# Kernel tuning notes

Hardware: AMD Instinct MI355X
Metric: run time of the kernel (lower is better)

## Reference

```python
import jax, jax.numpy as jnp
import numpy as np

N_QUBITS = 10
T_STEPS = 10
NDATA = 1024
DIM = 2 ** N_QUBITS
PI = float(np.pi)


def setup_inputs() -> dict:
    key = jax.random.key(0)
    k1, k2, k3, k4, k5 = jax.random.split(key, 5)
    # random complex amplitudes (normalized to unit states inside reference)
    inputs_re = jax.random.normal(k1, (NDATA, DIM), dtype=jnp.float32)
    inputs_im = jax.random.normal(k2, (NDATA, DIM), dtype=jnp.float32)
    # diffusion noise schedule diff_hs (t,) in (0,1]
    diff_hs = jax.random.uniform(k5, (T_STEPS,), dtype=jnp.float32, minval=0.1, maxval=1.0)
    # var_1 = diff_hs.repeat(3n) in torch == tile -> index k scaled by diff_hs[k % t]
    var_1 = jnp.tile(diff_hs, 3 * N_QUBITS)                                  # (3*n*t,)
    phis = (jax.random.uniform(k3, (NDATA, 3 * N_QUBITS * T_STEPS), dtype=jnp.float32)
            * (PI / 4.0) - (PI / 8.0)) * var_1[None, :]
    gs = (jax.random.uniform(k4, (NDATA, T_STEPS), dtype=jnp.float32) * 0.2 + 0.4) * diff_hs[None, :]
    return {"inputs_re": inputs_re, "inputs_im": inputs_im, "phis": phis, "gs": gs}


def _apply_1q(psi, M, i):
    """Apply per-sample 2x2 gate M (B,2,2) on qubit i (qubit 0 = MSB) to psi (B, 2**n)."""
    left = 2 ** i
    right = 2 ** (N_QUBITS - 1 - i)
    s = psi.reshape(NDATA, left, 2, right)
    s = jnp.einsum('bxy,bayc->baxc', M, s)
    return s.reshape(NDATA, DIM)


def _scramble(inputs_re, inputs_im, phis, gs):
    n, t = N_QUBITS, T_STEPS
    psi = (inputs_re + 1j * inputs_im).astype(jnp.complex64)
    psi = psi / jnp.linalg.norm(psi, axis=1, keepdims=True)  # unit input states

    # precompute sum_{i<j} z_i z_j per basis state for the diagonal RZZ product
    idx = jnp.arange(DIM)
    bits = (idx[:, None] >> jnp.arange(n - 1, -1, -1)[None, :]) & 1  # (DIM, n), qubit0=MSB
    z = 1.0 - 2.0 * bits.astype(jnp.float32)
    zsum = z.sum(axis=1)
    pairsum = 0.5 * (zsum ** 2 - n)                                   # (DIM,)
    inv = 1.0 / (2.0 * np.sqrt(float(n)))

    for tt in range(t):
        base = 3 * n * tt
        for i in range(n):
            a = phis[:, base + i]            # first RZ angle
            th = phis[:, base + n + i]       # RY angle
            b = phis[:, base + 2 * n + i]    # second RZ angle
            c = jnp.cos(0.5 * th).astype(jnp.complex64)
            s = jnp.sin(0.5 * th).astype(jnp.complex64)
            ea_m = jnp.exp(-0.5j * a); ea_p = jnp.exp(0.5j * a)
            eb_m = jnp.exp(-0.5j * b); eb_p = jnp.exp(0.5j * b)
            # M = RZ(b) @ RY(th) @ RZ(a), per sample (B,2,2)
            M = jnp.stack([
                jnp.stack([eb_m * c * ea_m, -eb_m * s * ea_p], axis=-1),
                jnp.stack([eb_p * s * ea_m,  eb_p * c * ea_p], axis=-1),
            ], axis=-2)
            psi = _apply_1q(psi, M, i)
        # all RZZ(i,j, theta) gates are diagonal with shared theta -> single fused phase
        theta = (gs[:, tt] * inv).astype(jnp.complex64)
        psi = psi * jnp.exp(-0.5j * theta[:, None] * pairsum[None, :])
    return psi


def reference(inputs_re, inputs_im, phis, gs):
    psi = _scramble(inputs_re, inputs_im, phis, gs)
    return jnp.stack([psi.real, psi.imag])  # (2, Ndata, 2**n) float32
```

## Files before the change

### kernel.cpp

```cpp
#include <hip/hip_runtime.h>

#define NQ 10
#define TS 10
#define DIM 1024
#define ND 1024
#define NR 16


template<int CTRL>
__device__ __forceinline__ float dpp_full(float x) {
    const int xi = __float_as_int(x);
    return __int_as_float(__builtin_amdgcn_update_dpp(xi, xi, CTRL, 0xF, 0xF, false));
}
__device__ __forceinline__ float dpp_xor4(float x) {
    const int xi = __float_as_int(x);
    int q = __builtin_amdgcn_update_dpp(0, xi, 0x104, 0xF, 0x5, false);
    q     = __builtin_amdgcn_update_dpp(q, xi, 0x114, 0xF, 0xA, false);
    return __int_as_float(q);
}
template<int MASK>
__device__ __forceinline__ float lshuf(float x) {
    if constexpr (MASK == 1)      return dpp_full<0xB1>(x);
    else if constexpr (MASK == 2) return dpp_full<0x4E>(x);
    else if constexpr (MASK == 4) return dpp_xor4(x);
    else if constexpr (MASK == 8) return dpp_full<0x128>(x);
    else return __shfl_xor(x, MASK, 64);
}

template <int RB>
__device__ __forceinline__ void ry_r(float* Sr, float* Si, float c, float s) {
#pragma unroll
    for (int r0 = 0; r0 < NR; ++r0) {
        if (r0 & (1 << RB)) continue;
        const int r1 = r0 | (1 << RB);
        const float x0r = Sr[r0], x1r = Sr[r1];
        const float x0i = Si[r0], x1i = Si[r1];
        Sr[r0] = c * x0r - s * x1r;
        Sr[r1] = s * x0r + c * x1r;
        Si[r0] = c * x0i - s * x1i;
        Si[r1] = s * x0i + c * x1i;
    }
}
template <int MASK>
__device__ __forceinline__ void ry_lane(int lane, float* Sr, float* Si,
                                        float c, float s) {
    const float ss = (lane & MASK) ? s : -s;
    float qr[NR], qi[NR];
#pragma unroll
    for (int r = 0; r < NR; ++r) {
        qr[r] = lshuf<MASK>(Sr[r]);
        qi[r] = lshuf<MASK>(Si[r]);
    }
#pragma unroll
    for (int r = 0; r < NR; ++r) {
        Sr[r] = c * Sr[r] + ss * qr[r];
        Si[r] = c * Si[r] + ss * qi[r];
    }
}

__global__ __launch_bounds__(64, 1) void qsim_kernel(
    const float* __restrict__ re_in, const float* __restrict__ im_in,
    const float* __restrict__ phis, const float* __restrict__ gs,
    float* __restrict__ out)
{
    const int sample = blockIdx.x;
    const int lane = threadIdx.x;

    const float* pr_in = re_in + sample * DIM;
    const float* pi_in = im_in + sample * DIM;

    float Sr[NR], Si[NR];
#pragma unroll
    for (int r = 0; r < NR; ++r) {
        Sr[r] = pr_in[r * 64 + lane];
        Si[r] = pi_in[r * 64 + lane];
    }

    const float inv = 0.15811388300841897f;
    const float* gsp = gs + sample * TS;

    float nrm = 0.f;
#pragma unroll
    for (int r = 0; r < NR; ++r) nrm += Sr[r] * Sr[r] + Si[r] * Si[r];
#pragma unroll
    for (int off = 32; off >= 1; off >>= 1) nrm += __shfl_xor(nrm, off, 64);
    const float scl = rsqrtf(nrm);
#pragma unroll
    for (int r = 0; r < NR; ++r) { Sr[r] *= scl; Si[r] *= scl; }

    float ps[NR];
#pragma unroll
    for (int r = 0; r < NR; ++r) {
        const int idx = r * 64 + lane;
        const int z = NQ - 2 * __popc(idx);
        ps[r] = 0.5f * (float)(z * z - NQ);
    }
    float bl[6];
#pragma unroll
    for (int j = 0; j < 6; ++j) bl[j] = (float)((lane >> (5 - j)) & 1);

    const float* ph = phis + sample * (3 * NQ * TS);

    float bprev[NQ];
#pragma unroll
    for (int i = 0; i < NQ; ++i) bprev[i] = 0.f;
    float kk = 0.f;

    auto apply_diag = [&](const float* v, float kcur) {
        float sv = 0.f;
#pragma unroll
        for (int i = 0; i < NQ; ++i) sv += v[i];
        float wl = 0.f;
#pragma unroll
        for (int j = 0; j < 6; ++j) wl = fmaf(bl[j], v[4 + j], wl);
        const float m = fmaf(-0.5f, sv, wl);
        const float Hm[4] = {m, m + v[1], m + v[0], m + v[0] + v[1]};
        const float L[4]  = {0.f, v[3], v[2], v[2] + v[3]};
#pragma unroll
        for (int r = 0; r < NR; ++r) {
            const float phi = fmaf(kcur, ps[r], Hm[r >> 2] + L[r & 3]);
            float sp, cp;
            __sincosf(phi, &sp, &cp);
            const float xr = Sr[r], xi = Si[r];
            Sr[r] = cp * xr - sp * xi;
            Si[r] = sp * xr + cp * xi;
        }
    };

    for (int tt = 0; tt < TS; ++tt) {
        float phs[30];
#pragma unroll
        for (int j = 0; j < 30; ++j) phs[j] = ph[30 * tt + j];

        float v[NQ];
#pragma unroll
        for (int i = 0; i < NQ; ++i) v[i] = phs[i] + bprev[i];
        apply_diag(v, kk);

        float rc[NQ], rs[NQ];
#pragma unroll
        for (int i = 0; i < NQ; ++i) __sincosf(0.5f * phs[10 + i], &rs[i], &rc[i]);

        ry_r<3>(Sr, Si, rc[0], rs[0]);
        ry_r<2>(Sr, Si, rc[1], rs[1]);
        ry_r<1>(Sr, Si, rc[2], rs[2]);
        ry_r<0>(Sr, Si, rc[3], rs[3]);
        ry_lane<32>(lane, Sr, Si, rc[4], rs[4]);
        ry_lane<16>(lane, Sr, Si, rc[5], rs[5]);
        ry_lane< 8>(lane, Sr, Si, rc[6], rs[6]);
        ry_lane< 4>(lane, Sr, Si, rc[7], rs[7]);
        ry_lane< 2>(lane, Sr, Si, rc[8], rs[8]);
        ry_lane< 1>(lane, Sr, Si, rc[9], rs[9]);

#pragma unroll
        for (int i = 0; i < NQ; ++i) bprev[i] = phs[20 + i];
        kk = -0.5f * (gsp[tt] * inv);
    }

    apply_diag(bprev, kk);

    float* outr = out + sample * DIM;
    float* outi = out + ND * DIM + sample * DIM;
#pragma unroll
    for (int r = 0; r < NR; ++r) {
        outr[r * 64 + lane] = Sr[r];
        outi[r * 64 + lane] = Si[r];
    }
}

extern "C" void kernel_launch(void* const* d_in, const int* in_sizes, int n_in,
                              void* d_out, int out_size, void* d_ws, size_t ws_size,
                              hipStream_t stream) {
    const float* re_in = (const float*)d_in[0];
    const float* im_in = (const float*)d_in[1];
    const float* phis  = (const float*)d_in[2];
    const float* gs    = (const float*)d_in[3];
    float* out = (float*)d_out;
    qsim_kernel<<<ND, 64, 0, stream>>>(re_in, im_in, phis, gs, out);
}
```

Before: 92.54 us.

## Apply RY gate layers as fp16 MFMA Kronecker-product matmuls

Replaces the per-qubit butterfly RY updates (register pairs plus DPP/shuffle lane exchanges) with two stages of 16x16x16 fp16 MFMA products. The first stage applies the tensor product of gates on qubits 0-3 and the second applies gates 4-9. The state is re-laid out to fit the MFMA fragment format, so the DPP/shuffle traffic goes away. The cost is fp16 rounding of the state and gate entries at every step, which may break accuracy tolerance, plus the work of building the gate matrices per lane.

```diff
diff --git a/kernel.cpp b/kernel.cpp
--- a/kernel.cpp
+++ b/kernel.cpp
@@ -4,58 +4,21 @@
 #define TS 10
 #define DIM 1024
 #define ND 1024
-#define NR 16
-
-
-template<int CTRL>
-__device__ __forceinline__ float dpp_full(float x) {
-    const int xi = __float_as_int(x);
-    return __int_as_float(__builtin_amdgcn_update_dpp(xi, xi, CTRL, 0xF, 0xF, false));
-}
-__device__ __forceinline__ float dpp_xor4(float x) {
-    const int xi = __float_as_int(x);
-    int q = __builtin_amdgcn_update_dpp(0, xi, 0x104, 0xF, 0x5, false);
-    q     = __builtin_amdgcn_update_dpp(q, xi, 0x114, 0xF, 0xA, false);
-    return __int_as_float(q);
-}
-template<int MASK>
-__device__ __forceinline__ float lshuf(float x) {
-    if constexpr (MASK == 1)      return dpp_full<0xB1>(x);
-    else if constexpr (MASK == 2) return dpp_full<0x4E>(x);
-    else if constexpr (MASK == 4) return dpp_xor4(x);
-    else if constexpr (MASK == 8) return dpp_full<0x128>(x);
-    else return __shfl_xor(x, MASK, 64);
-}
-
-template <int RB>
-__device__ __forceinline__ void ry_r(float* Sr, float* Si, float c, float s) {
-#pragma unroll
-    for (int r0 = 0; r0 < NR; ++r0) {
-        if (r0 & (1 << RB)) continue;
-        const int r1 = r0 | (1 << RB);
-        const float x0r = Sr[r0], x1r = Sr[r1];
-        const float x0i = Si[r0], x1i = Si[r1];
-        Sr[r0] = c * x0r - s * x1r;
-        Sr[r1] = s * x0r + c * x1r;
-        Si[r0] = c * x0i - s * x1i;
-        Si[r1] = s * x0i + c * x1i;
-    }
-}
-template <int MASK>
-__device__ __forceinline__ void ry_lane(int lane, float* Sr, float* Si,
-                                        float c, float s) {
-    const float ss = (lane & MASK) ? s : -s;
-    float qr[NR], qi[NR];
-#pragma unroll
-    for (int r = 0; r < NR; ++r) {
-        qr[r] = lshuf<MASK>(Sr[r]);
-        qi[r] = lshuf<MASK>(Si[r]);
-    }
-#pragma unroll
-    for (int r = 0; r < NR; ++r) {
-        Sr[r] = c * Sr[r] + ss * qr[r];
-        Si[r] = c * Si[r] + ss * qi[r];
-    }
+
+typedef _Float16 h4 __attribute__((ext_vector_type(4)));
+typedef float f4 __attribute__((ext_vector_type(4)));
+
+__device__ __forceinline__ f4 mfma16(h4 a, h4 b, f4 c) {
+    return __builtin_amdgcn_mfma_f32_16x16x16f16(a, b, c, 0, 0, 0);
+}
+__device__ __forceinline__ h4 cvt_h4(f4 x) {
+    h4 r;
+    r[0] = (_Float16)x[0]; r[1] = (_Float16)x[1];
+    r[2] = (_Float16)x[2]; r[3] = (_Float16)x[3];
+    return r;
+}
+__device__ __forceinline__ float hsel(int ob, int ib, float cq, float sq) {
+    return (ob == ib) ? cq : (ob ? sq : -sq);
 }
 
 __global__ __launch_bounds__(64, 1) void qsim_kernel(
@@ -65,41 +28,54 @@
 {
     const int sample = blockIdx.x;
     const int lane = threadIdx.x;
+    const int quad = lane >> 4;
+    const int cc = lane & 15;
+    const int c3 = (cc >> 3) & 1, c2 = (cc >> 2) & 1, c1 = (cc >> 1) & 1, c0 = cc & 1;
+    const int q1 = quad >> 1, q0 = quad & 1;
 
     const float* pr_in = re_in + sample * DIM;
     const float* pi_in = im_in + sample * DIM;
-
-    float Sr[NR], Si[NR];
-#pragma unroll
-    for (int r = 0; r < NR; ++r) {
-        Sr[r] = pr_in[r * 64 + lane];
-        Si[r] = pi_in[r * 64 + lane];
-    }
+    const float* ph = phis + sample * (3 * NQ * TS);
+    const float* gsp = gs + sample * TS;
+
+    f4 Sr[4], Si[4];
+    const int lbase = 256 * quad + cc;
+#pragma unroll
+    for (int n = 0; n < 4; ++n)
+#pragma unroll
+        for (int s = 0; s < 4; ++s) {
+            Sr[n][s] = pr_in[lbase + 64 * s + 16 * n];
+            Si[n][s] = pi_in[lbase + 64 * s + 16 * n];
+        }
 
     const float inv = 0.15811388300841897f;
-    const float* gsp = gs + sample * TS;
+    float gk[TS];
+#pragma unroll
+    for (int t = 0; t < TS; ++t) gk[t] = -0.5f * (gsp[t] * inv);
 
     float nrm = 0.f;
 #pragma unroll
-    for (int r = 0; r < NR; ++r) nrm += Sr[r] * Sr[r] + Si[r] * Si[r];
+    for (int n = 0; n < 4; ++n)
+#pragma unroll
+        for (int s = 0; s < 4; ++s) nrm += Sr[n][s] * Sr[n][s] + Si[n][s] * Si[n][s];
 #pragma unroll
     for (int off = 32; off >= 1; off >>= 1) nrm += __shfl_xor(nrm, off, 64);
     const float scl = rsqrtf(nrm);
 #pragma unroll
-    for (int r = 0; r < NR; ++r) { Sr[r] *= scl; Si[r] *= scl; }
-
-    float ps[NR];
-#pragma unroll
-    for (int r = 0; r < NR; ++r) {
-        const int idx = r * 64 + lane;
-        const int z = NQ - 2 * __popc(idx);
-        ps[r] = 0.5f * (float)(z * z - NQ);
-    }
-    float bl[6];
-#pragma unroll
-    for (int j = 0; j < 6; ++j) bl[j] = (float)((lane >> (5 - j)) & 1);
-
-    const float* ph = phis + sample * (3 * NQ * TS);
+    for (int n = 0; n < 4; ++n) { Sr[n] *= scl; Si[n] *= scl; }
+
+    float psv[4][4];
+    const int pbase = __popc(quad) + __popc(cc);
+#pragma unroll
+    for (int n = 0; n < 4; ++n)
+#pragma unroll
+        for (int s = 0; s < 4; ++s) {
+            const int p = pbase + __popc(n) + __popc(s);
+            const int z = NQ - 2 * p;
+            psv[n][s] = 0.5f * (float)(z * z - NQ);
+        }
+    const float fq1 = (float)q1, fq0 = (float)q0;
+    const float fc3 = (float)c3, fc2 = (float)c2, fc1 = (float)c1, fc0 = (float)c0;
 
     float bprev[NQ];
 #pragma unroll
@@ -110,22 +86,26 @@
         float sv = 0.f;
 #pragma unroll
         for (int i = 0; i < NQ; ++i) sv += v[i];
-        float wl = 0.f;
-#pragma unroll
-        for (int j = 0; j < 6; ++j) wl = fmaf(bl[j], v[4 + j], wl);
-        const float m = fmaf(-0.5f, sv, wl);
-        const float Hm[4] = {m, m + v[1], m + v[0], m + v[0] + v[1]};
-        const float L[4]  = {0.f, v[3], v[2], v[2] + v[3]};
-#pragma unroll
-        for (int r = 0; r < NR; ++r) {
-            const float phi = fmaf(kcur, ps[r], Hm[r >> 2] + L[r & 3]);
-            float sp, cp;
-            __sincosf(phi, &sp, &cp);
-            const float xr = Sr[r], xi = Si[r];
-            Sr[r] = cp * xr - sp * xi;
-            Si[r] = sp * xr + cp * xi;
-        }
+        float base = fmaf(-0.5f, sv, 0.f);
+        base = fmaf(fq1, v[0], base); base = fmaf(fq0, v[1], base);
+        base = fmaf(fc3, v[6], base); base = fmaf(fc2, v[7], base);
+        base = fmaf(fc1, v[8], base); base = fmaf(fc0, v[9], base);
+        const float addS[4] = {0.f, v[3], v[2], v[2] + v[3]};
+        const float addN[4] = {0.f, v[5], v[4], v[4] + v[5]};
+#pragma unroll
+        for (int n = 0; n < 4; ++n)
+#pragma unroll
+            for (int s = 0; s < 4; ++s) {
+                const float phi = fmaf(kcur, psv[n][s], base + addN[n] + addS[s]);
+                const float sp = __sinf(phi);
+                const float cp = __cosf(phi);
+                const float xr = Sr[n][s], xi = Si[n][s];
+                Sr[n][s] = cp * xr - sp * xi;
+                Si[n][s] = sp * xr + cp * xi;
+            }
     };
+
+    const f4 zf4 = {0.f, 0.f, 0.f, 0.f};
 
     for (int tt = 0; tt < TS; ++tt) {
         float phs[30];
@@ -137,24 +117,73 @@
         for (int i = 0; i < NQ; ++i) v[i] = phs[i] + bprev[i];
         apply_diag(v, kk);
 
-        float rc[NQ], rs[NQ];
-#pragma unroll
-        for (int i = 0; i < NQ; ++i) __sincosf(0.5f * phs[10 + i], &rs[i], &rc[i]);
-
-        ry_r<3>(Sr, Si, rc[0], rs[0]);
-        ry_r<2>(Sr, Si, rc[1], rs[1]);
-        ry_r<1>(Sr, Si, rc[2], rs[2]);
-        ry_r<0>(Sr, Si, rc[3], rs[3]);
-        ry_lane<32>(lane, Sr, Si, rc[4], rs[4]);
-        ry_lane<16>(lane, Sr, Si, rc[5], rs[5]);
-        ry_lane< 8>(lane, Sr, Si, rc[6], rs[6]);
-        ry_lane< 4>(lane, Sr, Si, rc[7], rs[7]);
-        ry_lane< 2>(lane, Sr, Si, rc[8], rs[8]);
-        ry_lane< 1>(lane, Sr, Si, rc[9], rs[9]);
+        float C[NQ], S[NQ];
+#pragma unroll
+        for (int g = 0; g < NQ; ++g) {
+            const float h = 0.5f * phs[10 + g];
+            S[g] = __sinf(h);
+            C[g] = __cosf(h);
+        }
+
+        h4 gb;
+        {
+            const float f01 = hsel(c3, q1, C[0], S[0]) * hsel(c2, q0, C[1], S[1]);
+#pragma unroll
+            for (int s = 0; s < 4; ++s) {
+                const float e = f01 * hsel(c1, s >> 1, C[2], S[2])
+                                    * hsel(c0, s & 1,  C[3], S[3]);
+                gb[s] = (_Float16)e;
+            }
+        }
+
+        h4 hb[4][4];
+        {
+            const float F67 = hsel(c3, q1, C[6], S[6]) * hsel(c2, q0, C[7], S[7]);
+            float F89[4];
+#pragma unroll
+            for (int s = 0; s < 4; ++s)
+                F89[s] = F67 * hsel(c1, s >> 1, C[8], S[8])
+                             * hsel(c0, s & 1,  C[9], S[9]);
+#pragma unroll
+            for (int n = 0; n < 4; ++n)
+#pragma unroll
+                for (int j = 0; j < 4; ++j) {
+                    const float F45 = hsel(n >> 1, j >> 1, C[4], S[4])
+                                    * hsel(n & 1,  j & 1,  C[5], S[5]);
+#pragma unroll
+                    for (int s = 0; s < 4; ++s)
+                        hb[n][j][s] = (_Float16)(F45 * F89[s]);
+                }
+        }
+
+        h4 ar[4], ai[4];
+#pragma unroll
+        for (int n = 0; n < 4; ++n) { ar[n] = cvt_h4(Sr[n]); ai[n] = cvt_h4(Si[n]); }
+        f4 Tr[4], Ti[4];
+#pragma unroll
+        for (int n = 0; n < 4; ++n) {
+            Tr[n] = mfma16(ar[n], gb, zf4);
+            Ti[n] = mfma16(ai[n], gb, zf4);
+        }
+        h4 tr[4], ti[4];
+#pragma unroll
+        for (int n = 0; n < 4; ++n) { tr[n] = cvt_h4(Tr[n]); ti[n] = cvt_h4(Ti[n]); }
+
+#pragma unroll
+        for (int n = 0; n < 4; ++n) {
+            f4 accr = zf4, acci = zf4;
+#pragma unroll
+            for (int j = 0; j < 4; ++j) {
+                accr = mfma16(tr[j], hb[n][j], accr);
+                acci = mfma16(ti[j], hb[n][j], acci);
+            }
+            Sr[n] = accr;
+            Si[n] = acci;
+        }
 
 #pragma unroll
         for (int i = 0; i < NQ; ++i) bprev[i] = phs[20 + i];
-        kk = -0.5f * (gsp[tt] * inv);
+        kk = gk[tt];
     }
 
     apply_diag(bprev, kk);
@@ -162,10 +191,12 @@
     float* outr = out + sample * DIM;
     float* outi = out + ND * DIM + sample * DIM;
 #pragma unroll
-    for (int r = 0; r < NR; ++r) {
-        outr[r * 64 + lane] = Sr[r];
-        outi[r * 64 + lane] = Si[r];
-    }
+    for (int n = 0; n < 4; ++n)
+#pragma unroll
+        for (int s = 0; s < 4; ++s) {
+            outr[lbase + 64 * s + 16 * n] = Sr[n][s];
+            outi[lbase + 64 * s + 16 * n] = Si[n][s];
+        }
 }
 
 extern "C" void kernel_launch(void* const* d_in, const int* in_sizes, int n_in,
```

After: 80.10 us. 13.4% less time.
